# Kernel optimization log

Hardware: AMD Instinct MI355X
Metric: run time of the kernel (lower is better)

The kernel has to match this reference:

```python
import jax, jax.numpy as jnp
import numpy as np

LN_EPS = 1e-5

def _layer_norm(x, gamma, beta):
    m = jnp.mean(x, axis=-1, keepdims=True)
    v = jnp.mean((x - m) ** 2, axis=-1, keepdims=True)
    return (x - m) / jnp.sqrt(v + LN_EPS) * gamma + beta

def setup_inputs() -> dict:
    key = jax.random.key(0)
    k1, k2, k3 = jax.random.split(key, 3)
    N, E, D = 8192, 4096, 128
    node_embeddings = jax.random.normal(k1, (N, D), dtype=jnp.float32)
    target_matrix = jax.random.normal(k2, (N, N), dtype=jnp.float32)
    hypergraph_matrix = jax.random.randint(k3, (N, E), 0, 2, dtype=jnp.int32)
    ln_gamma = jnp.ones((D,), dtype=jnp.float32)
    ln_beta = jnp.zeros((D,), dtype=jnp.float32)
    return {
        "node_embeddings": node_embeddings,
        "target_matrix": target_matrix,
        "ln_gamma": ln_gamma,
        "ln_beta": ln_beta,
        "hypergraph_matrix": hypergraph_matrix,
        "num_layers": 3,
    }

def reference(node_embeddings, target_matrix, ln_gamma, ln_beta, hypergraph_matrix, num_layers):
    x = node_embeddings  # [N, D]
    for _ in range(num_layers):
        t = jnp.matmul(target_matrix, x)        # [N, D]
        x = jnp.matmul(target_matrix.T, t)      # [N, D]
        x = _layer_norm(x, ln_gamma, ln_beta)
        # dropout is identity in eval mode
    # per-hyperedge masked mean over nodes, vectorized as a dense GEMV-style reduce
    h = (hypergraph_matrix > 0).astype(x.dtype)            # [N, E]
    counts = jnp.sum(h, axis=0)                            # [E]
    sums = jnp.einsum('ne,nd->ed', h, x)                   # [E, D]
    means = sums / counts[:, None]                         # [E, D]
    return jnp.max(means, axis=0)                          # [D]
```

## Files before the change

### kernel.cpp

```cpp
#include <hip/hip_runtime.h>
#include <cstdint>
#include <cstddef>

typedef __attribute__((ext_vector_type(8))) short short8;
typedef __attribute__((ext_vector_type(4))) short short4v;
typedef __attribute__((ext_vector_type(4))) float float4v;
typedef __attribute__((ext_vector_type(4))) int int4v;
typedef unsigned short ushort_t;

__device__ __forceinline__ ushort_t f2bf(float f) {
  unsigned u = __builtin_bit_cast(unsigned, f);
  u = (u + 0x7FFFu + ((u >> 16) & 1u)) >> 16;
  return (ushort_t)u;
}
__device__ __forceinline__ float bf2f(ushort_t h) {
  unsigned u = ((unsigned)h) << 16;
  return __builtin_bit_cast(float, u);
}

__device__ __forceinline__ void gld_lds16(const void* g, void* l) {
  __builtin_amdgcn_global_load_lds(
      (const __attribute__((address_space(1))) void*)g,
      (__attribute__((address_space(3))) void*)l, 16, 0, 0);
}


__global__ __launch_bounds__(256, 3) void gemm_tn(
    const ushort_t* __restrict__ A, const ushort_t* __restrict__ B,
    float* __restrict__ P, int M, int N, int K, int ATILED, int BTILED) {
  __shared__ ushort_t As[128 * 64];
  __shared__ ushort_t Bs[128 * 64];
  const int tid = threadIdx.x;
  const int lane = tid & 63;
  const int wave = tid >> 6;
  const int wm = (wave & 1) * 64;
  const int wn = (wave >> 1) * 64;
  const int m0 = blockIdx.x * 128;
  const int n0 = blockIdx.y * 128;
  int t0, tl;
  if (blockIdx.z < 8) { t0 = blockIdx.z * 11; tl = 11; }
  else { t0 = 88 + (blockIdx.z - 8) * 10; tl = 10; }
  float* __restrict__ Pc = P + (size_t)blockIdx.z * M * N;

  const char* aP[4];
  const char* bP[4];
  size_t aStep, bStep;
#pragma unroll
  for (int i = 0; i < 4; i++) {
    const int f = i * 4096 + tid * 16;
    if (ATILED) {
      aP[i] = (const char*)A +
              (((size_t)((m0 >> 6) + (f >> 13)) * (size_t)(K >> 6)) << 13) +
              (f & 8191);
    } else {
      aP[i] = (const char*)A + ((size_t)(m0 + (f >> 7)) * K) * 2 + (f & 127);
    }
    if (BTILED) {
      bP[i] = (const char*)B +
              (((size_t)((n0 >> 6) + (f >> 13)) * (size_t)(K >> 6)) << 13) +
              (f & 8191);
    } else {
      bP[i] = (const char*)B + ((size_t)(n0 + (f >> 7)) * K) * 2 + (f & 127);
    }
  }
  aStep = ATILED ? 8192 : 128;
  bStep = BTILED ? 8192 : 128;

  float4v acc[4][4] = {};

  for (int t = t0; t < t0 + tl; t++) {
#pragma unroll
    for (int i = 0; i < 4; i++) {
      const int f = i * 4096 + tid * 16;
      gld_lds16(aP[i] + (size_t)t * aStep, (char*)As + f);
      gld_lds16(bP[i] + (size_t)t * bStep, (char*)Bs + f);
    }
    __syncthreads();
#pragma unroll
    for (int ks = 0; ks < 64; ks += 32) {
      short8 af[4], bfr[4];
      const int kr = ks + (lane >> 4) * 8;
      const int l15 = lane & 15;
#pragma unroll
      for (int im = 0; im < 4; im++)
        af[im] = *(const short8*)&As[(wm + im * 16 + l15) * 64 + kr];
#pragma unroll
      for (int in = 0; in < 4; in++)
        bfr[in] = *(const short8*)&Bs[(wn + in * 16 + l15) * 64 + kr];
#pragma unroll
      for (int im = 0; im < 4; im++)
#pragma unroll
        for (int in = 0; in < 4; in++)
          acc[im][in] = __builtin_amdgcn_mfma_f32_16x16x32_bf16(
              af[im], bfr[in], acc[im][in], 0, 0, 0);
    }
    __syncthreads();
  }
  const int cn = lane & 15;
  const int cr = (lane >> 4) * 4;
#pragma unroll
  for (int im = 0; im < 4; im++)
#pragma unroll
    for (int in = 0; in < 4; in++)
#pragma unroll
      for (int r = 0; r < 4; r++) {
        int m = wm + im * 16 + cr + r;
        int n = wn + in * 16 + cn;
        Pc[(size_t)(m0 + m) * N + (n0 + n)] = acc[im][in][r];
      }
}

__global__ __launch_bounds__(256, 3) void gemm_nn(
    const ushort_t* __restrict__ A, const ushort_t* __restrict__ B,
    float* __restrict__ P, int M, int N, int K) {
  __shared__ ushort_t As[128 * 64];
  __shared__ ushort_t Bs[64 * 128];
  const int tid = threadIdx.x;
  const int lane = tid & 63;
  const int wave = tid >> 6;
  const int wm = (wave & 1) * 64;
  const int wn = (wave >> 1) * 64;
  const int m0 = blockIdx.x * 128;
  const int n0 = blockIdx.y * 128;
  int t0, tl;
  if (blockIdx.z < 8) { t0 = blockIdx.z * 11; tl = 11; }
  else { t0 = 88 + (blockIdx.z - 8) * 10; tl = 10; }
  float* __restrict__ Pc = P + (size_t)blockIdx.z * M * N;

  const char* aP[4];
  const char* bP[4];
#pragma unroll
  for (int i = 0; i < 4; i++) {
    const int c = i * 256 + tid;
    const int f = i * 4096 + tid * 16;
    const int brow = ((c >> 6) << 2) | ((c >> 1) & 3);
    const int bcol = (((c >> 3) & 7) << 4) | ((c & 1) << 3);
    const int bsrc = (bcol & 64 ? 8192 : 0) + brow * 128 + (bcol & 63) * 2;
    bP[i] = (const char*)B + ((size_t)(n0 >> 6) << 13) + bsrc;
    aP[i] = (const char*)A + ((size_t)(m0 + (f >> 7)) * K) * 2 + (f & 127);
  }
  const size_t bStep = (size_t)(N >> 6) << 13;

  const int l15 = lane & 15;
  const int hi = lane >> 4;
  const unsigned BsB =
      (unsigned)(uintptr_t)(__attribute__((address_space(3))) void*)Bs;
  const unsigned trb = BsB + (unsigned)(hi * 2048) + (unsigned)(l15 * 8);

  float4v acc[4][4] = {};

  for (int t = t0; t < t0 + tl; t++) {
#pragma unroll
    for (int i = 0; i < 4; i++) {
      const int f = i * 4096 + tid * 16;
      gld_lds16(aP[i] + (size_t)t * 128, (char*)As + f);
      gld_lds16(bP[i] + (size_t)t * bStep, (char*)Bs + f);
    }
    __syncthreads();
#pragma unroll
    for (int ks = 0; ks < 64; ks += 32) {
      short8 af[4];
      const int kr = ks + hi * 8;
#pragma unroll
      for (int im = 0; im < 4; im++)
        af[im] = *(const short8*)&As[(wm + im * 16 + l15) * 64 + kr];
      short4v r0[4], r1[4];
      const unsigned tb = trb + (unsigned)((ks >> 2) * 1024) + (unsigned)(wn * 8);
#pragma unroll
      for (int in = 0; in < 4; in++) {
        asm volatile(
            "ds_read_b64_tr_b16 %0, %2\n\t"
            "ds_read_b64_tr_b16 %1, %2 offset:1024"
            : "=&v"(r0[in]), "=&v"(r1[in])
            : "v"(tb + (unsigned)(in * 128)));
      }
      asm volatile("s_waitcnt lgkmcnt(0)" ::: "memory");
      __builtin_amdgcn_sched_barrier(0);
#pragma unroll
      for (int im = 0; im < 4; im++)
#pragma unroll
        for (int in = 0; in < 4; in++) {
          short8 bf8 = __builtin_shufflevector(r0[in], r1[in],
                                               0, 1, 2, 3, 4, 5, 6, 7);
          acc[im][in] = __builtin_amdgcn_mfma_f32_16x16x32_bf16(
              af[im], bf8, acc[im][in], 0, 0, 0);
        }
    }
    __syncthreads();
  }
  const int cn = lane & 15;
  const int cr = (lane >> 4) * 4;
#pragma unroll
  for (int im = 0; im < 4; im++)
#pragma unroll
    for (int in = 0; in < 4; in++)
#pragma unroll
      for (int r = 0; r < 4; r++) {
        int m = wm + im * 16 + cr + r;
        int n = wn + in * 16 + cn;
        Pc[(size_t)(m0 + m) * N + (n0 + n)] = acc[im][in][r];
      }
}

__global__ __launch_bounds__(256) void repack_T_k(
    const float* __restrict__ src, ushort_t* __restrict__ dst) {
  __shared__ ushort_t tile[32][520];
  const int bx = blockIdx.x;
  const int by = blockIdx.y;
  const int t = threadIdx.x;
  const int r = t >> 3, cs = (t & 7) * 64;
  const float* s = src + (size_t)(by * 32 + r) * 8192 + bx * 512 + cs;
#pragma unroll
  for (int j = 0; j < 64; j += 4) {
    float4v v = *(const float4v*)(s + j);
    short4v o;
    o.x = (short)f2bf(v.x); o.y = (short)f2bf(v.y);
    o.z = (short)f2bf(v.z); o.w = (short)f2bf(v.w);
    *(short4v*)&tile[r][cs + j] = o;
  }
  __syncthreads();
  const int q = t & 7;
  ushort_t* d = dst + ((size_t)(by >> 1) * 128 + bx * 8) * 4096 +
                (size_t)(by & 1) * 2048 + r * 64 + q * 8;
#pragma unroll
  for (int jj = 0; jj < 8; jj++)
    *(short8*)(d + (size_t)jj * 4096) = *(const short8*)&tile[r][jj * 64 + q * 8];
}

__global__ __launch_bounds__(256) void dualcast_f32_k(
    const float* __restrict__ src, ushort_t* __restrict__ dstN,
    ushort_t* __restrict__ dstT, int R, int C) {
  __shared__ float tile[64][65];
  const int c0 = blockIdx.x * 64, r0 = blockIdx.y * 64;
  const int tr = threadIdx.x >> 2, cs = (threadIdx.x & 3) * 16;
  const float* s = src + (size_t)(r0 + tr) * C + c0 + cs;
  float v[16];
#pragma unroll
  for (int j = 0; j < 16; j += 4) {
    float4v t4 = *(const float4v*)(s + j);
    v[j] = t4.x; v[j + 1] = t4.y; v[j + 2] = t4.z; v[j + 3] = t4.w;
  }
  if (dstN) {
    ushort_t o[16];
#pragma unroll
    for (int j = 0; j < 16; j++) o[j] = f2bf(v[j]);
    ushort_t* d = dstN + (size_t)(r0 + tr) * C + c0 + cs;
    *(short8*)d = *(const short8*)&o[0];
    *(short8*)(d + 8) = *(const short8*)&o[8];
  }
#pragma unroll
  for (int j = 0; j < 16; j++) tile[tr][cs + j] = v[j];
  __syncthreads();
  const int tc = threadIdx.x >> 2, rs = (threadIdx.x & 3) * 16;
  ushort_t o[16];
#pragma unroll
  for (int j = 0; j < 16; j++) o[j] = f2bf(tile[rs + j][tc]);
  ushort_t* d = dstT + (size_t)(c0 + tc) * R + r0 + rs;
  *(short8*)d = *(const short8*)&o[0];
  *(short8*)(d + 8) = *(const short8*)&o[8];
}

__global__ __launch_bounds__(256) void tcast_i32_k(
    const int* __restrict__ src, ushort_t* __restrict__ dstT,
    float* __restrict__ partial, int R, int C) {
  __shared__ float tile[64][65];
  const int c0 = blockIdx.x * 64, r0 = blockIdx.y * 64;
  const int tr = threadIdx.x >> 2, cs = (threadIdx.x & 3) * 16;
  const int* s = src + (size_t)(r0 + tr) * C + c0 + cs;
#pragma unroll
  for (int j = 0; j < 16; j += 4) {
    int4v t4 = *(const int4v*)(s + j);
    tile[tr][cs + j] = t4.x > 0 ? 1.f : 0.f;
    tile[tr][cs + j + 1] = t4.y > 0 ? 1.f : 0.f;
    tile[tr][cs + j + 2] = t4.z > 0 ? 1.f : 0.f;
    tile[tr][cs + j + 3] = t4.w > 0 ? 1.f : 0.f;
  }
  __syncthreads();
  const int tc = threadIdx.x >> 2, rs = (threadIdx.x & 3) * 16;
  ushort_t o[16];
#pragma unroll
  for (int j = 0; j < 16; j++) o[j] = f2bf(tile[rs + j][tc]);
  ushort_t* d = dstT + (((size_t)(c0 >> 6) * (size_t)(R >> 6) + (r0 >> 6)) << 12) +
                tc * 64 + rs;
  *(short8*)d = *(const short8*)&o[0];
  *(short8*)(d + 8) = *(const short8*)&o[8];
  if (threadIdx.x < 64) {
    float sum = 0.f;
#pragma unroll
    for (int r = 0; r < 64; r++) sum += tile[r][threadIdx.x];
    partial[(size_t)(r0 >> 6) * C + c0 + threadIdx.x] = sum;
  }
}

__global__ __launch_bounds__(256) void counts2_k(
    const float* __restrict__ partial, float* __restrict__ counts, int E) {
  const int e = blockIdx.x * 256 + threadIdx.x;
  float s = 0.f;
  for (int r = 0; r < 128; r++) s += partial[(size_t)r * E + e];
  counts[e] = s;
}

__global__ __launch_bounds__(256) void cast_k(
    const float* __restrict__ P, ushort_t* __restrict__ out, int MN) {
  const int i = (blockIdx.x * 256 + threadIdx.x) * 8;
  float4v a = {0.f, 0.f, 0.f, 0.f}, b = {0.f, 0.f, 0.f, 0.f};
  for (int sp = 0; sp < 12; sp++) {
    a += *(const float4v*)&P[(size_t)sp * MN + i];
    b += *(const float4v*)&P[(size_t)sp * MN + i + 4];
  }
  ushort_t o[8];
  o[0] = f2bf(a.x); o[1] = f2bf(a.y); o[2] = f2bf(a.z); o[3] = f2bf(a.w);
  o[4] = f2bf(b.x); o[5] = f2bf(b.y); o[6] = f2bf(b.z); o[7] = f2bf(b.w);
  *(short8*)&out[i] = *(const short8*)o;
}

__global__ __launch_bounds__(256) void ln_cast_k(
    const float* __restrict__ P, const float* __restrict__ gamma,
    const float* __restrict__ beta, ushort_t* __restrict__ xT, int Ncols) {
  __shared__ float ssum[8][32], ssq[8][32];
  const int c = threadIdx.x & 31;
  const int q = threadIdx.x >> 5;
  const int m = blockIdx.x * 32 + c;
  const size_t DN = (size_t)128 * Ncols;
  float vloc[16];
  float s = 0.f, sq = 0.f;
#pragma unroll
  for (int j = 0; j < 16; j++) {
    const int d = q * 16 + j;
    float v = 0.f;
    for (int sp = 0; sp < 12; sp++)
      v += P[(size_t)sp * DN + (size_t)d * Ncols + m];
    vloc[j] = v; s += v; sq += v * v;
  }
  ssum[q][c] = s;
  ssq[q][c] = sq;
  __syncthreads();
  float S = 0.f, SQ = 0.f;
#pragma unroll
  for (int r = 0; r < 8; r++) { S += ssum[r][c]; SQ += ssq[r][c]; }
  const float mean = S * (1.f / 128.f);
  const float var = SQ * (1.f / 128.f) - mean * mean;
  const float inv = rsqrtf(var + 1e-5f);
#pragma unroll
  for (int j = 0; j < 16; j++) {
    const int d = q * 16 + j;
    xT[(size_t)d * Ncols + m] = f2bf((vloc[j] - mean) * inv * gamma[d] + beta[d]);
  }
}

__global__ __launch_bounds__(256) void mm1_k(
    const float* __restrict__ P, const float* __restrict__ counts,
    float* __restrict__ pm, int EMN) {
  __shared__ float4v red[8][32];
  const int el = threadIdx.x >> 5;
  const int l32 = threadIdx.x & 31;
  const int e0 = blockIdx.x * 16;
  float4v vmax = {-3.4e38f, -3.4e38f, -3.4e38f, -3.4e38f};
  for (int ee = el; ee < 16; ee += 8) {
    const int e = e0 + ee;
    float4v s = {0.f, 0.f, 0.f, 0.f};
    for (int sp = 0; sp < 12; sp++)
      s += *(const float4v*)&P[(size_t)sp * EMN + (size_t)e * 128 + l32 * 4];
    const float inv = 1.f / counts[e];
    s *= inv;
    vmax.x = fmaxf(vmax.x, s.x); vmax.y = fmaxf(vmax.y, s.y);
    vmax.z = fmaxf(vmax.z, s.z); vmax.w = fmaxf(vmax.w, s.w);
  }
  red[el][l32] = vmax;
  __syncthreads();
  if (el == 0) {
    float4v m = red[0][l32];
#pragma unroll
    for (int r = 1; r < 8; r++) {
      float4v t = red[r][l32];
      m.x = fmaxf(m.x, t.x); m.y = fmaxf(m.y, t.y);
      m.z = fmaxf(m.z, t.z); m.w = fmaxf(m.w, t.w);
    }
    *(float4v*)&pm[(size_t)blockIdx.x * 128 + l32 * 4] = m;
  }
}

__global__ __launch_bounds__(128) void mm2_k(
    const float* __restrict__ pm, float* __restrict__ out, int B) {
  const int d = threadIdx.x;
  float v = -3.4e38f;
  for (int b = 0; b < B; b++) v = fmaxf(v, pm[b * 128 + d]);
  out[d] = v;
}

extern "C" void kernel_launch(void* const* d_in, const int* in_sizes, int n_in,
                              void* d_out, int out_size, void* d_ws,
                              size_t ws_size, hipStream_t stream) {
  const float* x0 = (const float*)d_in[0];
  const float* T = (const float*)d_in[1];
  const float* gamma = (const float*)d_in[2];
  const float* beta = (const float*)d_in[3];
  const int* h = (const int*)d_in[4];
  float* out = (float*)d_out;

  const int N = 8192, E = 4096, D = 128, K = 8192, S = 12;

  char* ws = (char*)d_ws;
  size_t off = 0;
  auto alloc = [&](size_t bytes) {
    char* p = ws + off;
    off += (bytes + 255) & ~(size_t)255;
    return p;
  };
  ushort_t* Tb = (ushort_t*)alloc((size_t)N * N * 2);
  ushort_t* hT = (ushort_t*)alloc((size_t)E * N * 2);
  ushort_t* xT = (ushort_t*)alloc((size_t)D * N * 2);
  ushort_t* tT = (ushort_t*)alloc((size_t)D * N * 2);
  float* P = (float*)alloc((size_t)S * D * N * 4);
  float* counts = (float*)alloc((size_t)E * 4);
  float* partial = (float*)alloc((size_t)(N / 64) * E * 4);
  float* pm = (float*)alloc((size_t)256 * D * 4);
  (void)ws_size;

  repack_T_k<<<dim3(16, 256), 256, 0, stream>>>(T, Tb);
  dualcast_f32_k<<<dim3(D / 64, N / 64), 256, 0, stream>>>(x0, nullptr, xT, N, D);
  tcast_i32_k<<<dim3(E / 64, N / 64), 256, 0, stream>>>(h, hT, partial, N, E);
  counts2_k<<<E / 256, 256, 0, stream>>>(partial, counts, E);

  for (int layer = 0; layer < 3; layer++) {
    gemm_tn<<<dim3(1, N / 128, S), 256, 0, stream>>>(xT, Tb, P, D, N, K, 0, 1);
    cast_k<<<D * N / (256 * 8), 256, 0, stream>>>(P, tT, D * N);
    gemm_nn<<<dim3(1, N / 128, S), 256, 0, stream>>>(tT, Tb, P, D, N, K);
    ln_cast_k<<<N / 32, 256, 0, stream>>>(P, gamma, beta, xT, N);
  }
  gemm_tn<<<dim3(E / 128, 1, S), 256, 0, stream>>>(hT, xT, P, E, D, K, 1, 0);
  mm1_k<<<E / 16, 256, 0, stream>>>(P, counts, pm, E * D);
  mm2_k<<<1, 128, 0, stream>>>(pm, out, E / 16);
}
```

Measured before the change: 824.3 us.

## Use 16 uniform split-K slices, 32-bit offsets, and fuse counts into mean-max

The split-K factor for all GEMMs goes from 12 uneven slices to 16 slices of exactly 8 K-tiles each, and launch bounds rise to 4 blocks per SM. Per-thread 64-bit pointer arrays become 32-bit offsets to save registers and allow the higher occupancy. The separate hyperedge count kernel is removed and its reduction is folded into mm1_k through shared memory. The cost is more partial-sum traffic in the cast, LayerNorm and reduction kernels, which now read 16 slices instead of 12.

Measured after the change: 842.9 us. 2.3% more time.

```diff
diff --git a/kernel.cpp b/kernel.cpp
--- a/kernel.cpp
+++ b/kernel.cpp
@@ -24,8 +24,10 @@
       (__attribute__((address_space(3))) void*)l, 16, 0, 0);
 }
 
-
-__global__ __launch_bounds__(256, 3) void gemm_tn(
+#define NSLICE 16
+
+
+__global__ __launch_bounds__(256, 4) void gemm_tn(
     const ushort_t* __restrict__ A, const ushort_t* __restrict__ B,
     float* __restrict__ P, int M, int N, int K, int ATILED, int BTILED) {
   __shared__ ushort_t As[128 * 64];
@@ -37,43 +39,35 @@
   const int wn = (wave >> 1) * 64;
   const int m0 = blockIdx.x * 128;
   const int n0 = blockIdx.y * 128;
-  int t0, tl;
-  if (blockIdx.z < 8) { t0 = blockIdx.z * 11; tl = 11; }
-  else { t0 = 88 + (blockIdx.z - 8) * 10; tl = 10; }
+  const int t0 = blockIdx.z * 8;
   float* __restrict__ Pc = P + (size_t)blockIdx.z * M * N;
 
-  const char* aP[4];
-  const char* bP[4];
-  size_t aStep, bStep;
+  unsigned aOff[4], bOff[4];
 #pragma unroll
   for (int i = 0; i < 4; i++) {
     const int f = i * 4096 + tid * 16;
-    if (ATILED) {
-      aP[i] = (const char*)A +
-              (((size_t)((m0 >> 6) + (f >> 13)) * (size_t)(K >> 6)) << 13) +
-              (f & 8191);
-    } else {
-      aP[i] = (const char*)A + ((size_t)(m0 + (f >> 7)) * K) * 2 + (f & 127);
-    }
-    if (BTILED) {
-      bP[i] = (const char*)B +
-              (((size_t)((n0 >> 6) + (f >> 13)) * (size_t)(K >> 6)) << 13) +
-              (f & 8191);
-    } else {
-      bP[i] = (const char*)B + ((size_t)(n0 + (f >> 7)) * K) * 2 + (f & 127);
-    }
-  }
-  aStep = ATILED ? 8192 : 128;
-  bStep = BTILED ? 8192 : 128;
+    aOff[i] = ATILED
+        ? ((unsigned)((m0 >> 6) + (f >> 13)) * (unsigned)(K >> 6)) * 8192u +
+              (unsigned)(f & 8191)
+        : (unsigned)(m0 + (f >> 7)) * (unsigned)K * 2u + (unsigned)(f & 127);
+    bOff[i] = BTILED
+        ? ((unsigned)((n0 >> 6) + (f >> 13)) * (unsigned)(K >> 6)) * 8192u +
+              (unsigned)(f & 8191)
+        : (unsigned)(n0 + (f >> 7)) * (unsigned)K * 2u + (unsigned)(f & 127);
+  }
+  const unsigned aStep = ATILED ? 8192u : 128u;
+  const unsigned bStep = BTILED ? 8192u : 128u;
 
   float4v acc[4][4] = {};
 
-  for (int t = t0; t < t0 + tl; t++) {
+  for (int t = t0; t < t0 + 8; t++) {
 #pragma unroll
     for (int i = 0; i < 4; i++) {
       const int f = i * 4096 + tid * 16;
-      gld_lds16(aP[i] + (size_t)t * aStep, (char*)As + f);
-      gld_lds16(bP[i] + (size_t)t * bStep, (char*)Bs + f);
+      gld_lds16((const char*)A + (size_t)(aOff[i] + (unsigned)t * aStep),
+                (char*)As + f);
+      gld_lds16((const char*)B + (size_t)(bOff[i] + (unsigned)t * bStep),
+                (char*)Bs + f);
     }
     __syncthreads();
 #pragma unroll
@@ -110,7 +104,7 @@
       }
 }
 
-__global__ __launch_bounds__(256, 3) void gemm_nn(
+__global__ __launch_bounds__(256, 4) void gemm_nn(
     const ushort_t* __restrict__ A, const ushort_t* __restrict__ B,
     float* __restrict__ P, int M, int N, int K) {
   __shared__ ushort_t As[128 * 64];
@@ -122,24 +116,21 @@
   const int wn = (wave >> 1) * 64;
   const int m0 = blockIdx.x * 128;
   const int n0 = blockIdx.y * 128;
-  int t0, tl;
-  if (blockIdx.z < 8) { t0 = blockIdx.z * 11; tl = 11; }
-  else { t0 = 88 + (blockIdx.z - 8) * 10; tl = 10; }
+  const int t0 = blockIdx.z * 8;
   float* __restrict__ Pc = P + (size_t)blockIdx.z * M * N;
 
-  const char* aP[4];
-  const char* bP[4];
+  unsigned aOff[4], bOff[4];
 #pragma unroll
   for (int i = 0; i < 4; i++) {
     const int c = i * 256 + tid;
     const int f = i * 4096 + tid * 16;
     const int brow = ((c >> 6) << 2) | ((c >> 1) & 3);
     const int bcol = (((c >> 3) & 7) << 4) | ((c & 1) << 3);
-    const int bsrc = (bcol & 64 ? 8192 : 0) + brow * 128 + (bcol & 63) * 2;
-    bP[i] = (const char*)B + ((size_t)(n0 >> 6) << 13) + bsrc;
-    aP[i] = (const char*)A + ((size_t)(m0 + (f >> 7)) * K) * 2 + (f & 127);
-  }
-  const size_t bStep = (size_t)(N >> 6) << 13;
+    bOff[i] = ((unsigned)(n0 >> 6) << 13) +
+              (unsigned)((bcol & 64 ? 8192 : 0) + brow * 128 + (bcol & 63) * 2);
+    aOff[i] = (unsigned)(m0 + (f >> 7)) * (unsigned)K * 2u + (unsigned)(f & 127);
+  }
+  const unsigned bStep = (unsigned)(N >> 6) << 13;
 
   const int l15 = lane & 15;
   const int hi = lane >> 4;
@@ -149,12 +140,14 @@
 
   float4v acc[4][4] = {};
 
-  for (int t = t0; t < t0 + tl; t++) {
+  for (int t = t0; t < t0 + 8; t++) {
 #pragma unroll
     for (int i = 0; i < 4; i++) {
       const int f = i * 4096 + tid * 16;
-      gld_lds16(aP[i] + (size_t)t * 128, (char*)As + f);
-      gld_lds16(bP[i] + (size_t)t * bStep, (char*)Bs + f);
+      gld_lds16((const char*)A + (size_t)(aOff[i] + (unsigned)t * 128u),
+                (char*)As + f);
+      gld_lds16((const char*)B + (size_t)(bOff[i] + (unsigned)t * bStep),
+                (char*)Bs + f);
     }
     __syncthreads();
 #pragma unroll
@@ -292,19 +285,11 @@
   }
 }
 
-__global__ __launch_bounds__(256) void counts2_k(
-    const float* __restrict__ partial, float* __restrict__ counts, int E) {
-  const int e = blockIdx.x * 256 + threadIdx.x;
-  float s = 0.f;
-  for (int r = 0; r < 128; r++) s += partial[(size_t)r * E + e];
-  counts[e] = s;
-}
-
 __global__ __launch_bounds__(256) void cast_k(
     const float* __restrict__ P, ushort_t* __restrict__ out, int MN) {
   const int i = (blockIdx.x * 256 + threadIdx.x) * 8;
   float4v a = {0.f, 0.f, 0.f, 0.f}, b = {0.f, 0.f, 0.f, 0.f};
-  for (int sp = 0; sp < 12; sp++) {
+  for (int sp = 0; sp < NSLICE; sp++) {
     a += *(const float4v*)&P[(size_t)sp * MN + i];
     b += *(const float4v*)&P[(size_t)sp * MN + i + 4];
   }
@@ -328,7 +313,7 @@
   for (int j = 0; j < 16; j++) {
     const int d = q * 16 + j;
     float v = 0.f;
-    for (int sp = 0; sp < 12; sp++)
+    for (int sp = 0; sp < NSLICE; sp++)
       v += P[(size_t)sp * DN + (size_t)d * Ncols + m];
     vloc[j] = v; s += v; sq += v * v;
   }
@@ -349,19 +334,33 @@
 }
 
 __global__ __launch_bounds__(256) void mm1_k(
-    const float* __restrict__ P, const float* __restrict__ counts,
-    float* __restrict__ pm, int EMN) {
+    const float* __restrict__ P, const float* __restrict__ partial,
+    float* __restrict__ pm, int EMN, int E) {
+  __shared__ float scnt[16][9];
   __shared__ float4v red[8][32];
-  const int el = threadIdx.x >> 5;
-  const int l32 = threadIdx.x & 31;
+  const int t = threadIdx.x;
   const int e0 = blockIdx.x * 16;
+  if (t < 128) {
+    const int ee = t >> 3, pp = t & 7;
+    float s = 0.f;
+#pragma unroll
+    for (int r = 0; r < 16; r++)
+      s += partial[(size_t)(pp * 16 + r) * E + e0 + ee];
+    scnt[ee][pp] = s;
+  }
+  __syncthreads();
+  const int el = t >> 5;
+  const int l32 = t & 31;
   float4v vmax = {-3.4e38f, -3.4e38f, -3.4e38f, -3.4e38f};
   for (int ee = el; ee < 16; ee += 8) {
     const int e = e0 + ee;
     float4v s = {0.f, 0.f, 0.f, 0.f};
-    for (int sp = 0; sp < 12; sp++)
+    for (int sp = 0; sp < NSLICE; sp++)
       s += *(const float4v*)&P[(size_t)sp * EMN + (size_t)e * 128 + l32 * 4];
-    const float inv = 1.f / counts[e];
+    float cnt = 0.f;
+#pragma unroll
+    for (int p = 0; p < 8; p++) cnt += scnt[ee][p];
+    const float inv = 1.f / cnt;
     s *= inv;
     vmax.x = fmaxf(vmax.x, s.x); vmax.y = fmaxf(vmax.y, s.y);
     vmax.z = fmaxf(vmax.z, s.z); vmax.w = fmaxf(vmax.w, s.w);
@@ -372,9 +371,9 @@
     float4v m = red[0][l32];
 #pragma unroll
     for (int r = 1; r < 8; r++) {
-      float4v t = red[r][l32];
-      m.x = fmaxf(m.x, t.x); m.y = fmaxf(m.y, t.y);
-      m.z = fmaxf(m.z, t.z); m.w = fmaxf(m.w, t.w);
+      float4v t4 = red[r][l32];
+      m.x = fmaxf(m.x, t4.x); m.y = fmaxf(m.y, t4.y);
+      m.z = fmaxf(m.z, t4.z); m.w = fmaxf(m.w, t4.w);
     }
     *(float4v*)&pm[(size_t)blockIdx.x * 128 + l32 * 4] = m;
   }
@@ -398,7 +397,7 @@
   const int* h = (const int*)d_in[4];
   float* out = (float*)d_out;
 
-  const int N = 8192, E = 4096, D = 128, K = 8192, S = 12;
+  const int N = 8192, E = 4096, D = 128, K = 8192, S = NSLICE;
 
   char* ws = (char*)d_ws;
   size_t off = 0;
@@ -412,7 +411,6 @@
   ushort_t* xT = (ushort_t*)alloc((size_t)D * N * 2);
   ushort_t* tT = (ushort_t*)alloc((size_t)D * N * 2);
   float* P = (float*)alloc((size_t)S * D * N * 4);
-  float* counts = (float*)alloc((size_t)E * 4);
   float* partial = (float*)alloc((size_t)(N / 64) * E * 4);
   float* pm = (float*)alloc((size_t)256 * D * 4);
   (void)ws_size;
@@ -420,7 +418,6 @@
   repack_T_k<<<dim3(16, 256), 256, 0, stream>>>(T, Tb);
   dualcast_f32_k<<<dim3(D / 64, N / 64), 256, 0, stream>>>(x0, nullptr, xT, N, D);
   tcast_i32_k<<<dim3(E / 64, N / 64), 256, 0, stream>>>(h, hT, partial, N, E);
-  counts2_k<<<E / 256, 256, 0, stream>>>(partial, counts, E);
 
   for (int layer = 0; layer < 3; layer++) {
     gemm_tn<<<dim3(1, N / 128, S), 256, 0, stream>>>(xT, Tb, P, D, N, K, 0, 1);
@@ -429,6 +426,6 @@
     ln_cast_k<<<N / 32, 256, 0, stream>>>(P, gamma, beta, xT, N);
   }
   gemm_tn<<<dim3(E / 128, 1, S), 256, 0, stream>>>(hT, xT, P, E, D, K, 1, 0);
-  mm1_k<<<E / 16, 256, 0, stream>>>(P, counts, pm, E * D);
+  mm1_k<<<E / 16, 256, 0, stream>>>(P, partial, pm, E * D, E);
   mm2_k<<<1, 128, 0, stream>>>(pm, out, E / 16);
 }
```
